# Optimization experiments

Measured on AMD Instinct MI355X. Metric: run time of the kernel, lower is better.

The kernel has to match this reference:

```python
import jax, jax.numpy as jnp
import numpy as np

N = 100000      # nodes
E = 3200000     # edges (before self loops)
IN, H, OUT = 512, 256, 64
K = 10
TEMP = 1.5
EPS = 1e-5


def setup_inputs() -> dict:
    key = jax.random.key(0)
    ks = jax.random.split(key, 16)
    def lin(k, fan_in, fan_out):
        lim = 1.0 / np.sqrt(fan_in)
        kw, kb = jax.random.split(k)
        w = jax.random.uniform(kw, (fan_in, fan_out), jnp.float32, -lim, lim)
        b = jax.random.uniform(kb, (fan_out,), jnp.float32, -lim, lim)
        return w, b
    w1, b1 = lin(ks[0], IN, H)
    w2, b2 = lin(ks[1], H, H)
    w3, b3 = lin(ks[2], H, H)
    w4, b4 = lin(ks[3], H, OUT)
    return {
        "x": jax.random.normal(ks[4], (N, IN), jnp.float32),
        "edge_index": jax.random.randint(ks[5], (2, E), 0, N, jnp.int64),
        "w1": w1, "b1": b1, "g1": jnp.ones((H,), jnp.float32), "be1": jnp.zeros((H,), jnp.float32),
        "w2": w2, "b2": b2, "g2": jnp.ones((H,), jnp.float32), "be2": jnp.zeros((H,), jnp.float32),
        "w3": w3, "b3": b3, "g3": jnp.ones((H,), jnp.float32), "be3": jnp.zeros((H,), jnp.float32),
        "w4": w4, "b4": b4,
        "alpha": jnp.full((K + 1,), 1.0 / (K + 1), jnp.float32),
    }


def _bn(h, g, b):
    # batch-statistics BatchNorm1d (training-mode normalization, biased var)
    m = h.mean(axis=0)
    v = ((h - m) ** 2).mean(axis=0)
    return g * (h - m) * jax.lax.rsqrt(v + EPS) + b


def reference(x, edge_index, w1, b1, g1, be1, w2, b2, g2, be2,
              w3, b3, g3, be3, w4, b4, alpha):
    n = x.shape[0]
    # add self loops
    loop = jnp.arange(n, dtype=edge_index.dtype)
    row = jnp.concatenate([edge_index[0], loop])
    col = jnp.concatenate([edge_index[1], loop])
    # symmetric normalization D^{-1/2} A D^{-1/2} (degree counted on row)
    deg = jax.ops.segment_sum(jnp.ones_like(row, x.dtype), row, num_segments=n)
    dinv = jnp.where(deg > 0, jax.lax.rsqrt(deg), 0.0)
    norm = dinv[row] * dinv[col]  # [E+N]

    gelu = lambda h: jax.nn.gelu(h, approximate=False)
    x0 = gelu(_bn(x @ w1 + b1, g1, be1))
    x1 = gelu(_bn(x0 @ w2 + b2, g2, be2) + x0)   # dropout=identity (eval)
    x2 = gelu(_bn(x1 @ w3 + b3, g3, be3) + x1)
    h = x2 @ w4 + b4                              # [N, OUT]

    def step(carry, a):
        xt, acc = carry
        xt = jax.ops.segment_sum(norm[:, None] * xt[col], row, num_segments=n)
        return (xt, acc + a * xt), None

    (_, acc), _ = jax.lax.scan(step, (h, alpha[0] * h), alpha[1:])
    return acc / TEMP
```

## Files before the change

kernel.cpp:

```cpp
#include <hip/hip_runtime.h>
#include <math.h>

#define N_NODES 100000
#define N_IN 512
#define N_H 256
#define N_OUT 64
#define KHOP 10
#define EPS_BN 1e-5f
#define INV_TEMP (1.0f/1.5f)
#define TILE_W 25000

using half8  = __attribute__((ext_vector_type(8))) _Float16;
using half4  = __attribute__((ext_vector_type(4))) _Float16;
using floatx4 = __attribute__((ext_vector_type(4))) float;

struct ZPtrs { const _Float16* p[KHOP]; };


__global__ void init_kernel(int* __restrict__ cnt4, float* __restrict__ sums, int n4) {
    int i = blockIdx.x * blockDim.x + threadIdx.x;
    if (i < n4) cnt4[i] = 0;
    if (i < 2 * N_H) sums[i] = 0.f;
}

__global__ __launch_bounds__(256) void fused_pre_kernel(
    const int* __restrict__ ei, int* __restrict__ cnt4, unsigned short* __restrict__ pos,
    const float* __restrict__ w1, _Float16* __restrict__ w1T,
    const float* __restrict__ w2, _Float16* __restrict__ w2T,
    const float* __restrict__ w3, _Float16* __restrict__ w3T,
    const float* __restrict__ w4, _Float16* __restrict__ w4T,
    int E, int nbE) {
    int bid = blockIdx.x;
    int t = threadIdx.x;
    if (bid < nbE) {
        int i = bid * 256 + t;
        if (i < E) {
            int r = ei[i];
            int c = ei[E + i];
            pos[i] = (unsigned short)atomicAdd(&cnt4[(r << 2) + c / TILE_W], 1);
        }
        return;
    }
    bid -= nbE;
    if (bid < 512) {
        int i = bid * 256 + t;
        int k = i >> 8, n = i & 255;
        w1T[(size_t)n * 512 + k] = (_Float16)w1[i];
        return;
    }
    bid -= 512;
    if (bid < 256) {
        int i = bid * 256 + t;
        int k = i >> 8, n = i & 255;
        w2T[(size_t)n * 256 + k] = (_Float16)w2[i];
        return;
    }
    bid -= 256;
    if (bid < 256) {
        int i = bid * 256 + t;
        int k = i >> 8, n = i & 255;
        w3T[(size_t)n * 256 + k] = (_Float16)w3[i];
        return;
    }
    bid -= 256;
    {
        int i = bid * 256 + t;
        int k = i >> 6, n = i & 63;
        w4T[(size_t)n * 256 + k] = (_Float16)w4[i];
    }
}

__global__ void scan1_kernel(const int* __restrict__ cnt4, int* __restrict__ excl,
                             int* __restrict__ bsum, int n4) {
    __shared__ int sd[256];
    int t = threadIdx.x;
    int base = blockIdx.x * 1024 + t * 4;
    int v0 = 0, v1 = 0, v2 = 0, v3 = 0;
    if (base + 0 < n4) { int g = base + 0; v0 = cnt4[g] + (((g & 3) == ((g >> 2) / TILE_W)) ? 1 : 0); }
    if (base + 1 < n4) { int g = base + 1; v1 = cnt4[g] + (((g & 3) == ((g >> 2) / TILE_W)) ? 1 : 0); }
    if (base + 2 < n4) { int g = base + 2; v2 = cnt4[g] + (((g & 3) == ((g >> 2) / TILE_W)) ? 1 : 0); }
    if (base + 3 < n4) { int g = base + 3; v3 = cnt4[g] + (((g & 3) == ((g >> 2) / TILE_W)) ? 1 : 0); }
    int tot = v0 + v1 + v2 + v3;
    sd[t] = tot;
    __syncthreads();
    for (int off = 1; off < 256; off <<= 1) {
        int x = (t >= off) ? sd[t - off] : 0;
        __syncthreads();
        sd[t] += x;
        __syncthreads();
    }
    int run = sd[t] - tot;
    if (t == 255) bsum[blockIdx.x] = sd[t];
    if (base + 0 < n4) excl[base + 0] = run; run += v0;
    if (base + 1 < n4) excl[base + 1] = run; run += v1;
    if (base + 2 < n4) excl[base + 2] = run; run += v2;
    if (base + 3 < n4) excl[base + 3] = run;
}

__global__ void scan2_kernel(int* __restrict__ bsum, int nb) {
    __shared__ int sd[512];
    int t = threadIdx.x;
    int v = (t < nb) ? bsum[t] : 0;
    sd[t] = v;
    __syncthreads();
    for (int off = 1; off < 512; off <<= 1) {
        int x = (t >= off) ? sd[t - off] : 0;
        __syncthreads();
        sd[t] += x;
        __syncthreads();
    }
    if (t < nb) bsum[t] = sd[t] - v;
}

__global__ void scan3_kernel(int* __restrict__ rp4, const int* __restrict__ bsum,
                             const int* __restrict__ cnt4, float* __restrict__ dinv,
                             float* __restrict__ dinv2, float* __restrict__ sqd,
                             int* __restrict__ colv, int n4, int total) {
    int g = blockIdx.x * blockDim.x + threadIdx.x;
    if (g < n4) {
        int rpf = rp4[g] + bsum[g >> 10];
        rp4[g] = rpf;
        int r = g >> 2, t = g & 3;
        int cv = cnt4[g];
        if (t == r / TILE_W) colv[rpf + cv] = r;
        if (t == 0) {
            int4 c4 = *reinterpret_cast<const int4*>(&cnt4[g]);
            float d = (float)(c4.x + c4.y + c4.z + c4.w + 1);
            dinv[r]  = rsqrtf(d);
            dinv2[r] = 1.0f / d;
            sqd[r]   = sqrtf(d);
        }
    }
    if (g == 0) rp4[n4] = total;
}

__global__ void fill_kernel(const int* __restrict__ ei, const unsigned short* __restrict__ pos,
                            const int* __restrict__ rp4,
                            int* __restrict__ colv, int E, int r0, int r1) {
    int i = blockIdx.x * blockDim.x + threadIdx.x;
    if (i >= E) return;
    int r = ei[i];
    if (r < r0 || r >= r1) return;
    int c = ei[E + i];
    colv[rp4[(r << 2) + c / TILE_W] + pos[i]] = c;
}


#define GELU(u) (0.5f * (u) * (1.f + erff((u) * 0.70710678118654752f)))

template<int KDIM, int NDIM, int BN, int AMODE, bool STATS, bool WRITE_X, bool WRITE_Z, typename CT>
__global__ __launch_bounds__(256) void gemm_mfma_kernel(
    const void* __restrict__ Araw, const _Float16* __restrict__ BT,
    const float* __restrict__ bias, CT* __restrict__ C, int M,
    float* __restrict__ sums, const float* __restrict__ ab,
    const _Float16* __restrict__ res, _Float16* __restrict__ xout,
    const float* __restrict__ dinv, _Float16* __restrict__ z0) {
    constexpr int BM = 128;
    constexpr int LDK = 40;
    constexpr int WTN = BN / 32;
    constexpr int NB = BN / 64;
    __shared__ _Float16 As[BM * LDK];
    __shared__ _Float16 Bs[BN * LDK];
    __shared__ float cs[BN];
    __shared__ float cq[BN];
    int t = threadIdx.x;
    int mbase = blockIdx.y * BM;
    int nbase = blockIdx.x * BN;
    int wv = t >> 6, lane = t & 63;
    int wm = (wv & 1) * 64;
    int wn = (wv >> 1) * (BN / 2);
    int q = lane >> 4;
    int fr = lane & 15;
    int sr = t >> 2;
    int sc = (t & 3) * 8;
    bool xwrite = WRITE_X && (blockIdx.x == 0);
    bool mok[2] = { mbase + sr < M, mbase + sr + 64 < M };

    floatx4 acc[4][WTN];
    for (int mt = 0; mt < 4; ++mt)
        for (int nt = 0; nt < WTN; ++nt)
            acc[mt][nt] = floatx4{0.f, 0.f, 0.f, 0.f};

    half8  aH[2];
    float4 aF[2][2];
    half8  rH[2];
    half8  bR[NB];

    auto issue_loads = [&](int kc) {
        #pragma unroll
        for (int p = 0; p < 2; ++p) {
            int grow = mbase + sr + p * 64;
            if (mok[p]) {
                if constexpr (AMODE == 1) {
                    const float* Af = (const float*)Araw + (size_t)grow * KDIM + kc;
                    aF[p][0] = *reinterpret_cast<const float4*>(Af);
                    aF[p][1] = *reinterpret_cast<const float4*>(Af + 4);
                } else {
                    aH[p] = *reinterpret_cast<const half8*>(
                        &((const _Float16*)Araw)[(size_t)grow * KDIM + kc]);
                    if constexpr (AMODE == 3)
                        rH[p] = *reinterpret_cast<const half8*>(&res[(size_t)grow * KDIM + kc]);
                }
            }
        }
        #pragma unroll
        for (int p = 0; p < NB; ++p)
            bR[p] = *reinterpret_cast<const half8*>(
                &BT[(size_t)(nbase + sr + p * 64) * KDIM + kc]);
    };

    issue_loads(sc);

    for (int k0 = 0; k0 < KDIM; k0 += 32) {
        int kc = k0 + sc;
        #pragma unroll
        for (int p = 0; p < 2; ++p) {
            int row = sr + p * 64;
            int grow = mbase + row;
            half8 v = {};
            if (mok[p]) {
                if constexpr (AMODE == 0) {
                    v = aH[p];
                } else if constexpr (AMODE == 1) {
                    v[0] = (_Float16)aF[p][0].x; v[1] = (_Float16)aF[p][0].y;
                    v[2] = (_Float16)aF[p][0].z; v[3] = (_Float16)aF[p][0].w;
                    v[4] = (_Float16)aF[p][1].x; v[5] = (_Float16)aF[p][1].y;
                    v[6] = (_Float16)aF[p][1].z; v[7] = (_Float16)aF[p][1].w;
                } else {
                    float4 a0 = *reinterpret_cast<const float4*>(&ab[kc]);
                    float4 a1 = *reinterpret_cast<const float4*>(&ab[kc + 4]);
                    float4 b0 = *reinterpret_cast<const float4*>(&ab[KDIM + kc]);
                    float4 b1 = *reinterpret_cast<const float4*>(&ab[KDIM + kc + 4]);
                    float u[8];
                    u[0] = a0.x * (float)aH[p][0] + b0.x;
                    u[1] = a0.y * (float)aH[p][1] + b0.y;
                    u[2] = a0.z * (float)aH[p][2] + b0.z;
                    u[3] = a0.w * (float)aH[p][3] + b0.w;
                    u[4] = a1.x * (float)aH[p][4] + b1.x;
                    u[5] = a1.y * (float)aH[p][5] + b1.y;
                    u[6] = a1.z * (float)aH[p][6] + b1.z;
                    u[7] = a1.w * (float)aH[p][7] + b1.w;
                    if constexpr (AMODE == 3) {
                        #pragma unroll
                        for (int j = 0; j < 8; ++j) u[j] += (float)rH[p][j];
                    }
                    #pragma unroll
                    for (int j = 0; j < 8; ++j) v[j] = (_Float16)GELU(u[j]);
                    if (xwrite)
                        *reinterpret_cast<half8*>(&xout[(size_t)grow * KDIM + kc]) = v;
                }
            }
            *reinterpret_cast<half8*>(&As[row * LDK + sc]) = v;
        }
        #pragma unroll
        for (int p = 0; p < NB; ++p)
            *reinterpret_cast<half8*>(&Bs[(sr + p * 64) * LDK + sc]) = bR[p];
        if (k0 + 32 < KDIM) issue_loads(kc + 32);
        __syncthreads();
        half8 af[4], bf[WTN];
        #pragma unroll
        for (int mt = 0; mt < 4; ++mt)
            af[mt] = *reinterpret_cast<const half8*>(&As[(wm + mt * 16 + fr) * LDK + q * 8]);
        #pragma unroll
        for (int nt = 0; nt < WTN; ++nt)
            bf[nt] = *reinterpret_cast<const half8*>(&Bs[(wn + nt * 16 + fr) * LDK + q * 8]);
        #pragma unroll
        for (int mt = 0; mt < 4; ++mt)
            #pragma unroll
            for (int nt = 0; nt < WTN; ++nt)
                acc[mt][nt] = __builtin_amdgcn_mfma_f32_16x16x32_f16(af[mt], bf[nt], acc[mt][nt], 0, 0, 0);
        __syncthreads();
    }
    if constexpr (STATS) {
        if (t < BN) { cs[t] = 0.f; cq[t] = 0.f; }
        __syncthreads();
    }
    #pragma unroll
    for (int nt = 0; nt < WTN; ++nt) {
        int col = nbase + wn + nt * 16 + fr;
        float bv = bias[col];
        float s = 0.f, s2 = 0.f;
        #pragma unroll
        for (int mt = 0; mt < 4; ++mt) {
            #pragma unroll
            for (int rr = 0; rr < 4; ++rr) {
                int row = mbase + wm + mt * 16 + q * 4 + rr;
                if (row < M) {
                    float v = acc[mt][nt][rr] + bv;
                    C[(size_t)row * NDIM + col] = (CT)v;
                    if constexpr (STATS) { s += v; s2 += v * v; }
                    if constexpr (WRITE_Z)
                        z0[((size_t)row << 6) + col] = (_Float16)(dinv[row] * v);
                }
            }
        }
        if constexpr (STATS) {
            s  += __shfl_xor(s, 16);  s  += __shfl_xor(s, 32);
            s2 += __shfl_xor(s2, 16); s2 += __shfl_xor(s2, 32);
            if (q == 0) {
                atomicAdd(&cs[wn + nt * 16 + fr], s);
                atomicAdd(&cq[wn + nt * 16 + fr], s2);
            }
        }
    }
    if constexpr (STATS) {
        __syncthreads();
        if (t < BN) {
            atomicAdd(&sums[nbase + t], cs[t]);
            atomicAdd(&sums[N_H + nbase + t], cq[t]);
        }
    }
}


__global__ void finalize_stats_kernel(float* __restrict__ sums,
                                      const float* __restrict__ g, const float* __restrict__ be,
                                      float* __restrict__ ab, float invM) {
    int c = threadIdx.x;
    float s = sums[c], s2 = sums[N_H + c];
    float mean = s * invM;
    float var = s2 * invM - mean * mean;
    float a = g[c] * rsqrtf(var + EPS_BN);
    ab[c] = a;
    ab[N_H + c] = be[c] - mean * a;
    sums[c] = 0.f;
    sums[N_H + c] = 0.f;
}


__global__ __launch_bounds__(256) void prop_kernel(
    const _Float16* __restrict__ zin, _Float16* __restrict__ zout,
    const int* __restrict__ colv, const int* __restrict__ rp4,
    const float* __restrict__ dinv2, int n) {
    int r = (blockIdx.x << 2) + (threadIdx.x >> 6);
    if (r >= n) return;
    int lane = threadIdx.x & 63;
    int esub = lane >> 4;
    int fo = (lane & 15) << 2;
    int s = __builtin_amdgcn_readfirstlane(rp4[r << 2]);
    int e = __builtin_amdgcn_readfirstlane(rp4[(r << 2) + 4]);
    float a0 = 0.f, a1 = 0.f, a2 = 0.f, a3 = 0.f;
    int i = s;
    for (; i + 32 <= e; i += 32) {
        int cc[8]; half4 vv[8];
        #pragma unroll
        for (int j = 0; j < 8; ++j) cc[j] = colv[i + 4 * j + esub];
        #pragma unroll
        for (int j = 0; j < 8; ++j)
            vv[j] = *reinterpret_cast<const half4*>(&zin[((size_t)cc[j] << 6) + fo]);
        #pragma unroll
        for (int j = 0; j < 8; ++j) {
            a0 += (float)vv[j].x; a1 += (float)vv[j].y;
            a2 += (float)vv[j].z; a3 += (float)vv[j].w;
        }
    }
    for (; i + 16 <= e; i += 16) {
        int cc[4]; half4 vv[4];
        #pragma unroll
        for (int j = 0; j < 4; ++j) cc[j] = colv[i + 4 * j + esub];
        #pragma unroll
        for (int j = 0; j < 4; ++j)
            vv[j] = *reinterpret_cast<const half4*>(&zin[((size_t)cc[j] << 6) + fo]);
        #pragma unroll
        for (int j = 0; j < 4; ++j) {
            a0 += (float)vv[j].x; a1 += (float)vv[j].y;
            a2 += (float)vv[j].z; a3 += (float)vv[j].w;
        }
    }
    for (; i + 4 <= e; i += 4) {
        int c = colv[i + esub];
        half4 v = *reinterpret_cast<const half4*>(&zin[((size_t)c << 6) + fo]);
        a0 += (float)v.x; a1 += (float)v.y; a2 += (float)v.z; a3 += (float)v.w;
    }
    if (esub < e - i) {
        int c = colv[i + esub];
        half4 v = *reinterpret_cast<const half4*>(&zin[((size_t)c << 6) + fo]);
        a0 += (float)v.x; a1 += (float)v.y; a2 += (float)v.z; a3 += (float)v.w;
    }
    a0 += __shfl_xor(a0, 16); a1 += __shfl_xor(a1, 16);
    a2 += __shfl_xor(a2, 16); a3 += __shfl_xor(a3, 16);
    a0 += __shfl_xor(a0, 32); a1 += __shfl_xor(a1, 32);
    a2 += __shfl_xor(a2, 32); a3 += __shfl_xor(a3, 32);
    if (lane < 16) {
        float d = dinv2[r];
        half4 o;
        o.x = (_Float16)(a0 * d); o.y = (_Float16)(a1 * d);
        o.z = (_Float16)(a2 * d); o.w = (_Float16)(a3 * d);
        *reinterpret_cast<half4*>(&zout[((size_t)r << 6) + fo]) = o;
    }
}

__global__ void prop_final_kernel(const float* __restrict__ h, ZPtrs zp,
                                  const float* __restrict__ sqd,
                                  const float* __restrict__ alpha,
                                  float* __restrict__ out, int total4) {
    int i = blockIdx.x * blockDim.x + threadIdx.x;
    if (i >= total4) return;
    int r = i >> 4;
    float4 hv = reinterpret_cast<const float4*>(h)[i];
    float s0 = 0.f, s1 = 0.f, s2 = 0.f, s3 = 0.f;
    #pragma unroll
    for (int k = 0; k < KHOP; ++k) {
        half4 z = reinterpret_cast<const half4*>(zp.p[k])[i];
        float ak = alpha[k + 1];
        s0 += ak * (float)z.x; s1 += ak * (float)z.y;
        s2 += ak * (float)z.z; s3 += ak * (float)z.w;
    }
    float sq = sqd[r];
    float a0 = alpha[0];
    float4 o;
    o.x = INV_TEMP * (a0 * hv.x + sq * s0);
    o.y = INV_TEMP * (a0 * hv.y + sq * s1);
    o.z = INV_TEMP * (a0 * hv.z + sq * s2);
    o.w = INV_TEMP * (a0 * hv.w + sq * s3);
    reinterpret_cast<float4*>(out)[i] = o;
}


extern "C" void kernel_launch(void* const* d_in, const int* in_sizes, int n_in,
                              void* d_out, int out_size, void* d_ws, size_t ws_size,
                              hipStream_t stream) {
    const float* x    = (const float*)d_in[0];
    const int*   ei   = (const int*)d_in[1];
    const float* w1   = (const float*)d_in[2];
    const float* b1   = (const float*)d_in[3];
    const float* g1   = (const float*)d_in[4];
    const float* be1  = (const float*)d_in[5];
    const float* w2   = (const float*)d_in[6];
    const float* b2   = (const float*)d_in[7];
    const float* g2   = (const float*)d_in[8];
    const float* be2  = (const float*)d_in[9];
    const float* w3   = (const float*)d_in[10];
    const float* b3   = (const float*)d_in[11];
    const float* g3   = (const float*)d_in[12];
    const float* be3  = (const float*)d_in[13];
    const float* w4   = (const float*)d_in[14];
    const float* b4   = (const float*)d_in[15];
    const float* alpha= (const float*)d_in[16];
    float* out = (float*)d_out;

    const int N = in_sizes[0] / N_IN;
    const int E = in_sizes[1] / 2;
    const int EN = E + N;
    const int N4 = N * 4;
    const size_t NZ = (size_t)N * N_OUT;

    char* ws = (char*)d_ws;
    size_t off = 0;
    auto alloc = [&](size_t bytes) -> void* {
        void* p = ws + off;
        off = (off + bytes + 255) & ~(size_t)255;
        return p;
    };
    int*   cnt4    = (int*)alloc((size_t)N4 * 4);
    int*   rp4     = (int*)alloc((size_t)(N4 + 1) * 4);
    float* dinv    = (float*)alloc((size_t)N * 4);
    float* dinv2   = (float*)alloc((size_t)N * 4);
    float* sqd     = (float*)alloc((size_t)N * 4);
    int*   colv    = (int*)alloc((size_t)EN * 4);
    unsigned short* pos = (unsigned short*)alloc((size_t)E * 2);
    int*   bsum    = (int*)alloc(512 * 4);
    float* sums    = (float*)alloc(2 * N_H * 4);
    float* ab      = (float*)alloc(2 * N_H * 4);
    _Float16* w1T  = (_Float16*)alloc((size_t)N_IN * N_H * 2);
    _Float16* w2T  = (_Float16*)alloc((size_t)N_H * N_H * 2);
    _Float16* w3T  = (_Float16*)alloc((size_t)N_H * N_H * 2);
    _Float16* w4T  = (_Float16*)alloc((size_t)N_H * N_OUT * 2);
    float* T       = (float*)alloc((size_t)N * N_H * 4);
    _Float16* Ah0  = (_Float16*)alloc((size_t)N * N_H * 2);
    _Float16* Ah1  = (_Float16*)alloc((size_t)N * N_H * 2);
    float* hbuf    = (float*)alloc((size_t)N * N_OUT * 4);
    _Float16* z0   = (_Float16*)alloc(NZ * 2);

    _Float16* T16a = (_Float16*)T;
    _Float16* T16b = (_Float16*)T + (size_t)N * N_H;

    _Float16* zk[KHOP + 1];
    zk[0] = z0;
    for (int k = 1; k <= 8; ++k) zk[k] = (_Float16*)T + (size_t)(k - 1) * NZ;
    zk[9]  = (_Float16*)Ah1;
    zk[10] = (_Float16*)Ah1 + NZ;

    const int TB = 256;
    int nbN4 = (N4 + TB - 1) / TB;
    int nbE  = (E + TB - 1) / TB;
    int nscan = (N4 + 1023) / 1024;

    init_kernel<<<nbN4, TB, 0, stream>>>(cnt4, sums, N4);
    {
        int grid = nbE + 512 + 256 + 256 + 64;
        fused_pre_kernel<<<grid, TB, 0, stream>>>(ei, cnt4, pos,
                                                  w1, w1T, w2, w2T, w3, w3T, w4, w4T,
                                                  E, nbE);
    }

    scan1_kernel<<<nscan, TB, 0, stream>>>(cnt4, rp4, bsum, N4);
    scan2_kernel<<<1, 512, 0, stream>>>(bsum, nscan);
    scan3_kernel<<<nbN4, TB, 0, stream>>>(rp4, bsum, cnt4, dinv, dinv2, sqd, colv, N4, EN);

    {
        const int P = 4;
        int step = (N + P - 1) / P;
        for (int p = 0; p < P; ++p) {
            int r0 = p * step;
            int r1 = min(N, r0 + step);
            fill_kernel<<<nbE, TB, 0, stream>>>(ei, pos, rp4, colv, E, r0, r1);
        }
    }

    int mt = (N + 127) / 128;

    gemm_mfma_kernel<N_IN, N_H, 128, 1, true, false, false, _Float16>
        <<<dim3(N_H / 128, mt), TB, 0, stream>>>(
        x, w1T, b1, T16a, N, sums, nullptr, nullptr, nullptr, nullptr, nullptr);
    finalize_stats_kernel<<<1, N_H, 0, stream>>>(sums, g1, be1, ab, 1.0f / N);
    gemm_mfma_kernel<N_H, N_H, 128, 2, true, true, false, _Float16>
        <<<dim3(N_H / 128, mt), TB, 0, stream>>>(
        T16a, w2T, b2, T16b, N, sums, ab, nullptr, Ah0, nullptr, nullptr);
    finalize_stats_kernel<<<1, N_H, 0, stream>>>(sums, g2, be2, ab, 1.0f / N);
    gemm_mfma_kernel<N_H, N_H, 128, 3, true, true, false, _Float16>
        <<<dim3(N_H / 128, mt), TB, 0, stream>>>(
        T16b, w3T, b3, T16a, N, sums, ab, Ah0, Ah1, nullptr, nullptr);
    finalize_stats_kernel<<<1, N_H, 0, stream>>>(sums, g3, be3, ab, 1.0f / N);
    gemm_mfma_kernel<N_H, N_OUT, 64, 3, false, false, true, float>
        <<<dim3(1, mt), TB, 0, stream>>>(
        T16a, w4T, b4, hbuf, N, nullptr, ab, Ah1, nullptr, dinv, z0);

    int nbProp = (N + 3) / 4;
    for (int k = 1; k <= KHOP; ++k) {
        prop_kernel<<<nbProp, TB, 0, stream>>>(zk[k - 1], zk[k], colv, rp4, dinv2, N);
    }

    ZPtrs zp;
    for (int k = 0; k < KHOP; ++k) zp.p[k] = zk[k + 1];
    int total4 = N * N_OUT / 4;
    prop_final_kernel<<<(total4 + TB - 1) / TB, TB, 0, stream>>>(hbuf, zp, sqd, alpha, out, total4);
}
```

Baseline: 1.532 ms.

## Co-schedule graph CSR build phases with MLP GEMMs in fused launches

Merges the edge-count atomic pass with the first GEMM into one launch, and folds the four partitioned CSR fill passes into the second and third GEMM launches, two buckets each. Weight transposes move into the init kernel. The aim is to overlap the memory- and atomic-bound graph preprocessing with the compute-bound MFMA GEMMs and to cut launch count. In exchange the GEMM blocks now share the machine with scatter blocks, and block scheduling order can delay the GEMM tail.

```diff
diff --git a/kernel.cpp b/kernel.cpp
--- a/kernel.cpp
+++ b/kernel.cpp
@@ -17,31 +17,21 @@
 struct ZPtrs { const _Float16* p[KHOP]; };
 
 
-__global__ void init_kernel(int* __restrict__ cnt4, float* __restrict__ sums, int n4) {
-    int i = blockIdx.x * blockDim.x + threadIdx.x;
-    if (i < n4) cnt4[i] = 0;
-    if (i < 2 * N_H) sums[i] = 0.f;
-}
-
-__global__ __launch_bounds__(256) void fused_pre_kernel(
-    const int* __restrict__ ei, int* __restrict__ cnt4, unsigned short* __restrict__ pos,
+__global__ __launch_bounds__(256) void init_kernel(
+    int* __restrict__ cnt4, float* __restrict__ sums, int n4, int nbN4,
     const float* __restrict__ w1, _Float16* __restrict__ w1T,
     const float* __restrict__ w2, _Float16* __restrict__ w2T,
     const float* __restrict__ w3, _Float16* __restrict__ w3T,
-    const float* __restrict__ w4, _Float16* __restrict__ w4T,
-    int E, int nbE) {
+    const float* __restrict__ w4, _Float16* __restrict__ w4T) {
     int bid = blockIdx.x;
     int t = threadIdx.x;
-    if (bid < nbE) {
+    if (bid < nbN4) {
         int i = bid * 256 + t;
-        if (i < E) {
-            int r = ei[i];
-            int c = ei[E + i];
-            pos[i] = (unsigned short)atomicAdd(&cnt4[(r << 2) + c / TILE_W], 1);
-        }
+        if (i < n4) cnt4[i] = 0;
+        if (i < 2 * N_H) sums[i] = 0.f;
         return;
     }
-    bid -= nbE;
+    bid -= nbN4;
     if (bid < 512) {
         int i = bid * 256 + t;
         int k = i >> 8, n = i & 255;
@@ -70,86 +60,12 @@
     }
 }
 
-__global__ void scan1_kernel(const int* __restrict__ cnt4, int* __restrict__ excl,
-                             int* __restrict__ bsum, int n4) {
-    __shared__ int sd[256];
-    int t = threadIdx.x;
-    int base = blockIdx.x * 1024 + t * 4;
-    int v0 = 0, v1 = 0, v2 = 0, v3 = 0;
-    if (base + 0 < n4) { int g = base + 0; v0 = cnt4[g] + (((g & 3) == ((g >> 2) / TILE_W)) ? 1 : 0); }
-    if (base + 1 < n4) { int g = base + 1; v1 = cnt4[g] + (((g & 3) == ((g >> 2) / TILE_W)) ? 1 : 0); }
-    if (base + 2 < n4) { int g = base + 2; v2 = cnt4[g] + (((g & 3) == ((g >> 2) / TILE_W)) ? 1 : 0); }
-    if (base + 3 < n4) { int g = base + 3; v3 = cnt4[g] + (((g & 3) == ((g >> 2) / TILE_W)) ? 1 : 0); }
-    int tot = v0 + v1 + v2 + v3;
-    sd[t] = tot;
-    __syncthreads();
-    for (int off = 1; off < 256; off <<= 1) {
-        int x = (t >= off) ? sd[t - off] : 0;
-        __syncthreads();
-        sd[t] += x;
-        __syncthreads();
-    }
-    int run = sd[t] - tot;
-    if (t == 255) bsum[blockIdx.x] = sd[t];
-    if (base + 0 < n4) excl[base + 0] = run; run += v0;
-    if (base + 1 < n4) excl[base + 1] = run; run += v1;
-    if (base + 2 < n4) excl[base + 2] = run; run += v2;
-    if (base + 3 < n4) excl[base + 3] = run;
-}
-
-__global__ void scan2_kernel(int* __restrict__ bsum, int nb) {
-    __shared__ int sd[512];
-    int t = threadIdx.x;
-    int v = (t < nb) ? bsum[t] : 0;
-    sd[t] = v;
-    __syncthreads();
-    for (int off = 1; off < 512; off <<= 1) {
-        int x = (t >= off) ? sd[t - off] : 0;
-        __syncthreads();
-        sd[t] += x;
-        __syncthreads();
-    }
-    if (t < nb) bsum[t] = sd[t] - v;
-}
-
-__global__ void scan3_kernel(int* __restrict__ rp4, const int* __restrict__ bsum,
-                             const int* __restrict__ cnt4, float* __restrict__ dinv,
-                             float* __restrict__ dinv2, float* __restrict__ sqd,
-                             int* __restrict__ colv, int n4, int total) {
-    int g = blockIdx.x * blockDim.x + threadIdx.x;
-    if (g < n4) {
-        int rpf = rp4[g] + bsum[g >> 10];
-        rp4[g] = rpf;
-        int r = g >> 2, t = g & 3;
-        int cv = cnt4[g];
-        if (t == r / TILE_W) colv[rpf + cv] = r;
-        if (t == 0) {
-            int4 c4 = *reinterpret_cast<const int4*>(&cnt4[g]);
-            float d = (float)(c4.x + c4.y + c4.z + c4.w + 1);
-            dinv[r]  = rsqrtf(d);
-            dinv2[r] = 1.0f / d;
-            sqd[r]   = sqrtf(d);
-        }
-    }
-    if (g == 0) rp4[n4] = total;
-}
-
-__global__ void fill_kernel(const int* __restrict__ ei, const unsigned short* __restrict__ pos,
-                            const int* __restrict__ rp4,
-                            int* __restrict__ colv, int E, int r0, int r1) {
-    int i = blockIdx.x * blockDim.x + threadIdx.x;
-    if (i >= E) return;
-    int r = ei[i];
-    if (r < r0 || r >= r1) return;
-    int c = ei[E + i];
-    colv[rp4[(r << 2) + c / TILE_W] + pos[i]] = c;
-}
-
 
 #define GELU(u) (0.5f * (u) * (1.f + erff((u) * 0.70710678118654752f)))
 
 template<int KDIM, int NDIM, int BN, int AMODE, bool STATS, bool WRITE_X, bool WRITE_Z, typename CT>
-__global__ __launch_bounds__(256) void gemm_mfma_kernel(
+__device__ __forceinline__ void gemm_body(
+    int bx, int by,
     const void* __restrict__ Araw, const _Float16* __restrict__ BT,
     const float* __restrict__ bias, CT* __restrict__ C, int M,
     float* __restrict__ sums, const float* __restrict__ ab,
@@ -164,8 +80,8 @@
     __shared__ float cs[BN];
     __shared__ float cq[BN];
     int t = threadIdx.x;
-    int mbase = blockIdx.y * BM;
-    int nbase = blockIdx.x * BN;
+    int mbase = by * BM;
+    int nbase = bx * BN;
     int wv = t >> 6, lane = t & 63;
     int wm = (wv & 1) * 64;
     int wn = (wv >> 1) * (BN / 2);
@@ -173,7 +89,7 @@
     int fr = lane & 15;
     int sr = t >> 2;
     int sc = (t & 3) * 8;
-    bool xwrite = WRITE_X && (blockIdx.x == 0);
+    bool xwrite = WRITE_X && (bx == 0);
     bool mok[2] = { mbase + sr < M, mbase + sr + 64 < M };
 
     floatx4 acc[4][WTN];
@@ -313,6 +229,134 @@
 }
 
 
+__global__ __launch_bounds__(256) void pre_g1_kernel(
+    const int* __restrict__ ei, int* __restrict__ cnt4, unsigned short* __restrict__ pos,
+    int E, int nbE,
+    const float* __restrict__ x, const _Float16* __restrict__ w1T,
+    const float* __restrict__ b1, _Float16* __restrict__ C, int M,
+    float* __restrict__ sums) {
+    int bid = blockIdx.x;
+    if (bid < nbE) {
+        int i = bid * 256 + threadIdx.x;
+        if (i < E) {
+            int r = ei[i];
+            int c = ei[E + i];
+            pos[i] = (unsigned short)atomicAdd(&cnt4[(r << 2) + c / TILE_W], 1);
+        }
+        return;
+    }
+    bid -= nbE;
+    gemm_body<N_IN, N_H, 128, 1, true, false, false, _Float16>(
+        bid & 1, bid >> 1, x, w1T, b1, C, M, sums,
+        nullptr, nullptr, nullptr, nullptr, nullptr);
+}
+
+
+template<int AMODE, bool WRITE_X>
+__global__ __launch_bounds__(256) void fill_g_kernel(
+    const int* __restrict__ ei, const unsigned short* __restrict__ pos,
+    const int* __restrict__ rp4, int* __restrict__ colv, int E, int nbE,
+    int bucket0, int step, int n,
+    const _Float16* __restrict__ A, const _Float16* __restrict__ BT,
+    const float* __restrict__ bias, _Float16* __restrict__ C, int M,
+    float* __restrict__ sums, const float* __restrict__ ab,
+    const _Float16* __restrict__ res, _Float16* __restrict__ xout) {
+    int bid = blockIdx.x;
+    if (bid < 2 * nbE) {
+        int p = bucket0 + (bid >= nbE ? 1 : 0);
+        int i = (bid >= nbE ? bid - nbE : bid) * 256 + threadIdx.x;
+        if (i < E) {
+            int r = ei[i];
+            int r0 = p * step, r1 = min(n, r0 + step);
+            if (r >= r0 && r < r1) {
+                int c = ei[E + i];
+                colv[rp4[(r << 2) + c / TILE_W] + pos[i]] = c;
+            }
+        }
+        return;
+    }
+    bid -= 2 * nbE;
+    gemm_body<N_H, N_H, 128, AMODE, true, WRITE_X, false, _Float16>(
+        bid & 1, bid >> 1, A, BT, bias, C, M, sums, ab, res, xout, nullptr, nullptr);
+}
+
+template<int KDIM, int NDIM, int BN, int AMODE, bool STATS, bool WRITE_X, bool WRITE_Z, typename CT>
+__global__ __launch_bounds__(256) void gemm_mfma_kernel(
+    const void* __restrict__ Araw, const _Float16* __restrict__ BT,
+    const float* __restrict__ bias, CT* __restrict__ C, int M,
+    float* __restrict__ sums, const float* __restrict__ ab,
+    const _Float16* __restrict__ res, _Float16* __restrict__ xout,
+    const float* __restrict__ dinv, _Float16* __restrict__ z0) {
+    gemm_body<KDIM, NDIM, BN, AMODE, STATS, WRITE_X, WRITE_Z, CT>(
+        blockIdx.x, blockIdx.y, Araw, BT, bias, C, M, sums, ab, res, xout, dinv, z0);
+}
+
+
+__global__ void scan1_kernel(const int* __restrict__ cnt4, int* __restrict__ excl,
+                             int* __restrict__ bsum, int n4) {
+    __shared__ int sd[256];
+    int t = threadIdx.x;
+    int base = blockIdx.x * 1024 + t * 4;
+    int v0 = 0, v1 = 0, v2 = 0, v3 = 0;
+    if (base + 0 < n4) { int g = base + 0; v0 = cnt4[g] + (((g & 3) == ((g >> 2) / TILE_W)) ? 1 : 0); }
+    if (base + 1 < n4) { int g = base + 1; v1 = cnt4[g] + (((g & 3) == ((g >> 2) / TILE_W)) ? 1 : 0); }
+    if (base + 2 < n4) { int g = base + 2; v2 = cnt4[g] + (((g & 3) == ((g >> 2) / TILE_W)) ? 1 : 0); }
+    if (base + 3 < n4) { int g = base + 3; v3 = cnt4[g] + (((g & 3) == ((g >> 2) / TILE_W)) ? 1 : 0); }
+    int tot = v0 + v1 + v2 + v3;
+    sd[t] = tot;
+    __syncthreads();
+    for (int off = 1; off < 256; off <<= 1) {
+        int x = (t >= off) ? sd[t - off] : 0;
+        __syncthreads();
+        sd[t] += x;
+        __syncthreads();
+    }
+    int run = sd[t] - tot;
+    if (t == 255) bsum[blockIdx.x] = sd[t];
+    if (base + 0 < n4) excl[base + 0] = run; run += v0;
+    if (base + 1 < n4) excl[base + 1] = run; run += v1;
+    if (base + 2 < n4) excl[base + 2] = run; run += v2;
+    if (base + 3 < n4) excl[base + 3] = run;
+}
+
+__global__ void scan2_kernel(int* __restrict__ bsum, int nb) {
+    __shared__ int sd[512];
+    int t = threadIdx.x;
+    int v = (t < nb) ? bsum[t] : 0;
+    sd[t] = v;
+    __syncthreads();
+    for (int off = 1; off < 512; off <<= 1) {
+        int x = (t >= off) ? sd[t - off] : 0;
+        __syncthreads();
+        sd[t] += x;
+        __syncthreads();
+    }
+    if (t < nb) bsum[t] = sd[t] - v;
+}
+
+__global__ void scan3_kernel(int* __restrict__ rp4, const int* __restrict__ bsum,
+                             const int* __restrict__ cnt4, float* __restrict__ dinv,
+                             float* __restrict__ dinv2, float* __restrict__ sqd,
+                             int* __restrict__ colv, int n4, int total) {
+    int g = blockIdx.x * blockDim.x + threadIdx.x;
+    if (g < n4) {
+        int rpf = rp4[g] + bsum[g >> 10];
+        rp4[g] = rpf;
+        int r = g >> 2, t = g & 3;
+        int cv = cnt4[g];
+        if (t == r / TILE_W) colv[rpf + cv] = r;
+        if (t == 0) {
+            int4 c4 = *reinterpret_cast<const int4*>(&cnt4[g]);
+            float d = (float)(c4.x + c4.y + c4.z + c4.w + 1);
+            dinv[r]  = rsqrtf(d);
+            dinv2[r] = 1.0f / d;
+            sqd[r]   = sqrtf(d);
+        }
+    }
+    if (g == 0) rp4[n4] = total;
+}
+
+
 __global__ void finalize_stats_kernel(float* __restrict__ sums,
                                       const float* __restrict__ g, const float* __restrict__ be,
                                       float* __restrict__ ab, float invM) {
@@ -485,43 +529,32 @@
     int nbN4 = (N4 + TB - 1) / TB;
     int nbE  = (E + TB - 1) / TB;
     int nscan = (N4 + 1023) / 1024;
-
-    init_kernel<<<nbN4, TB, 0, stream>>>(cnt4, sums, N4);
-    {
-        int grid = nbE + 512 + 256 + 256 + 64;
-        fused_pre_kernel<<<grid, TB, 0, stream>>>(ei, cnt4, pos,
-                                                  w1, w1T, w2, w2T, w3, w3T, w4, w4T,
-                                                  E, nbE);
-    }
+    int mt = (N + 127) / 128;
+    int g128 = 2 * mt;
+    int fstep = (N + 3) / 4;
+
+    init_kernel<<<nbN4 + 512 + 256 + 256 + 64, TB, 0, stream>>>(
+        cnt4, sums, N4, nbN4, w1, w1T, w2, w2T, w3, w3T, w4, w4T);
+
+    pre_g1_kernel<<<nbE + g128, TB, 0, stream>>>(
+        ei, cnt4, pos, E, nbE, x, w1T, b1, T16a, N, sums);
 
     scan1_kernel<<<nscan, TB, 0, stream>>>(cnt4, rp4, bsum, N4);
     scan2_kernel<<<1, 512, 0, stream>>>(bsum, nscan);
     scan3_kernel<<<nbN4, TB, 0, stream>>>(rp4, bsum, cnt4, dinv, dinv2, sqd, colv, N4, EN);
 
-    {
-        const int P = 4;
-        int step = (N + P - 1) / P;
-        for (int p = 0; p < P; ++p) {
-            int r0 = p * step;
-            int r1 = min(N, r0 + step);
-            fill_kernel<<<nbE, TB, 0, stream>>>(ei, pos, rp4, colv, E, r0, r1);
-        }
-    }
-
-    int mt = (N + 127) / 128;
-
-    gemm_mfma_kernel<N_IN, N_H, 128, 1, true, false, false, _Float16>
-        <<<dim3(N_H / 128, mt), TB, 0, stream>>>(
-        x, w1T, b1, T16a, N, sums, nullptr, nullptr, nullptr, nullptr, nullptr);
     finalize_stats_kernel<<<1, N_H, 0, stream>>>(sums, g1, be1, ab, 1.0f / N);
-    gemm_mfma_kernel<N_H, N_H, 128, 2, true, true, false, _Float16>
-        <<<dim3(N_H / 128, mt), TB, 0, stream>>>(
-        T16a, w2T, b2, T16b, N, sums, ab, nullptr, Ah0, nullptr, nullptr);
+
+    fill_g_kernel<2, true><<<2 * nbE + g128, TB, 0, stream>>>(
+        ei, pos, rp4, colv, E, nbE, 0, fstep, N,
+        T16a, w2T, b2, T16b, N, sums, ab, nullptr, Ah0);
     finalize_stats_kernel<<<1, N_H, 0, stream>>>(sums, g2, be2, ab, 1.0f / N);
-    gemm_mfma_kernel<N_H, N_H, 128, 3, true, true, false, _Float16>
-        <<<dim3(N_H / 128, mt), TB, 0, stream>>>(
-        T16b, w3T, b3, T16a, N, sums, ab, Ah0, Ah1, nullptr, nullptr);
+
+    fill_g_kernel<3, true><<<2 * nbE + g128, TB, 0, stream>>>(
+        ei, pos, rp4, colv, E, nbE, 2, fstep, N,
+        T16b, w3T, b3, T16a, N, sums, ab, Ah0, Ah1);
     finalize_stats_kernel<<<1, N_H, 0, stream>>>(sums, g3, be3, ab, 1.0f / N);
+
     gemm_mfma_kernel<N_H, N_OUT, 64, 3, false, false, true, float>
         <<<dim3(1, mt), TB, 0, stream>>>(
         T16a, w4T, b4, hbuf, N, nullptr, ab, Ah1, nullptr, dinv, z0);
```

Result: slower. 1.592 ms (+3.9%).
